# Performance work log

Measured on AMD Instinct MI355X. Metric: run time of the kernel, lower is better.

The kernel has to match this reference:

```python
import jax, jax.numpy as jnp
import numpy as np

GRID = 512
F_FEAT = 32
CORE = 16
N_PTS = 2097152
SCALE = 0.1


def _bilinear_sample(plane, coords):
    """plane: (F, H, W); coords: (N, 2) with (x, y) in [-1, 1], align_corners=True.
    Returns (F, N)."""
    F_, H, W = plane.shape
    x = (coords[:, 0] + 1.0) * 0.5 * (W - 1)
    y = (coords[:, 1] + 1.0) * 0.5 * (H - 1)
    x0f = jnp.floor(x)
    y0f = jnp.floor(y)
    wx = x - x0f  # (N,)
    wy = y - y0f
    x0 = jnp.clip(x0f.astype(jnp.int32), 0, W - 1)
    x1 = jnp.clip(x0 + 1, 0, W - 1)
    y0 = jnp.clip(y0f.astype(jnp.int32), 0, H - 1)
    y1 = jnp.clip(y0 + 1, 0, H - 1)
    v00 = plane[:, y0, x0]  # (F, N)
    v01 = plane[:, y0, x1]
    v10 = plane[:, y1, x0]
    v11 = plane[:, y1, x1]
    return (v00 * (1.0 - wx) * (1.0 - wy)
            + v01 * wx * (1.0 - wy)
            + v10 * (1.0 - wx) * wy
            + v11 * wx * wy)


def setup_inputs() -> dict:
    key = jax.random.key(0)
    k1, k2, k3, k4, k5 = jax.random.split(key, 5)
    coords_plane = jax.random.uniform(
        k1, (3, 1, N_PTS, 1, 2), dtype=jnp.float32, minval=-1.0, maxval=1.0)
    plane_xy = SCALE * jax.random.normal(k2, (1, F_FEAT, GRID, GRID), dtype=jnp.float32)
    plane_yz = SCALE * jax.random.normal(k3, (1, F_FEAT, GRID, GRID), dtype=jnp.float32)
    plane_xz = SCALE * jax.random.normal(k4, (1, F_FEAT, GRID, GRID), dtype=jnp.float32)
    core_tensor = jax.random.normal(k5, (CORE, F_FEAT), dtype=jnp.float32)
    return {"coords_plane": coords_plane, "plane_xy": plane_xy,
            "plane_yz": plane_yz, "plane_xz": plane_xz,
            "core_tensor": core_tensor}


def reference(coords_plane, plane_xy, plane_yz, plane_xz, core_tensor):
    # coords_plane: (3, 1, N, 1, 2) -> (3, N, 2)
    c = coords_plane.reshape(3, -1, 2)
    f_xy = _bilinear_sample(plane_xy[0], c[0])  # (F, N)
    f_yz = _bilinear_sample(plane_yz[0], c[1])
    f_xz = _bilinear_sample(plane_xz[0], c[2])
    prod = f_xy * f_yz * f_xz                   # (F, N)
    # sum over core dim: out[f, n] = (sum_k core[k, f]) * prod[f, n]
    scale = jnp.sum(core_tensor, axis=0)        # (F,)
    out = (scale[:, None] * prod).T             # (N, F)
    return out
```

## Files before the change

kernel.cpp:

```cpp
#include <hip/hip_runtime.h>
#include <hip/hip_fp16.h>

#define N_PTS 2097152
#define GRID_ 512
#define F_FEAT 32
#define HW (GRID_ * GRID_)
#define HWF ((size_t)HW * F_FEAT)

#define NBINS 64
#define BIN_SHIFT 3
#define BIN_CAP 36864
#define CUR_STRIDE 32
#define PTS_PER_BLOCK 1024
#define SEGCAP 64
#define BPB 288

typedef float f32x4 __attribute__((ext_vector_type(4)));
typedef unsigned long long u64;

__global__ void td_scale_kernel(const float* __restrict__ core,
                                float* __restrict__ scale) {
    int f = threadIdx.x;
    float s = 0.0f;
#pragma unroll
    for (int k = 0; k < 16; ++k) s += core[k * F_FEAT + f];
    scale[f] = s;
}

__global__ void td_transpose_kernel(const float* __restrict__ pxy,
                                    const float* __restrict__ pyz,
                                    const float* __restrict__ pxz,
                                    const float* __restrict__ scale,
                                    __half* __restrict__ wsh) {
    __shared__ float tile[32][33];
    const int plane = blockIdx.z;
    const float* src = (plane == 0) ? pxy : ((plane == 1) ? pyz : pxz);
    __half* dst = wsh + (size_t)plane * HWF;
    const int y = blockIdx.y;
    const int x0 = blockIdx.x * 32;

    for (int i = threadIdx.y; i < 32; i += 8) {
        tile[i][threadIdx.x] =
            src[(size_t)i * HW + (size_t)y * GRID_ + x0 + threadIdx.x];
    }
    __syncthreads();
    const float sc = (plane == 0) ? scale[threadIdx.x] : 1.0f;
    for (int i = threadIdx.y; i < 32; i += 8) {
        dst[((size_t)(y * GRID_ + x0 + i)) * F_FEAT + threadIdx.x] =
            __float2half(tile[threadIdx.x][i] * sc);
    }
}

__global__ void td_zero_kernel(int* __restrict__ cursor) {
    for (int i = threadIdx.x; i < 3 * NBINS * CUR_STRIDE; i += 256) cursor[i] = 0;
}

__global__ __launch_bounds__(256) void td_bin_kernel(
    const float2* __restrict__ coords, int* __restrict__ cursor,
    u64* __restrict__ recs) {
    __shared__ int lhist[NBINS];
    __shared__ int lbase[NBINS];
    __shared__ u64 lseg[NBINS][SEGCAP];
    const int pl = blockIdx.y;
    const int tid = threadIdx.x;
    const int base_p = blockIdx.x * PTS_PER_BLOCK;
    if (tid < NBINS) lhist[tid] = 0;
    __syncthreads();

    u64 myrec[4];
    int mybin[4], myslot[4];
#pragma unroll
    for (int k = 0; k < 4; ++k) {
        const int p = base_p + k * 256 + tid;
        const float2 c = coords[(size_t)pl * N_PTS + p];
        const float xf = (c.x + 1.0f) * 0.5f * (float)(GRID_ - 1);
        const float yf = (c.y + 1.0f) * 0.5f * (float)(GRID_ - 1);
        const float x0f = floorf(xf);
        const float y0f = floorf(yf);
        const float wx = xf - x0f;
        const float wy = yf - y0f;
        int x0 = min(max((int)x0f, 0), GRID_ - 1);
        int y0 = min(max((int)y0f, 0), GRID_ - 1);
        const int qwx = min(4095, (int)(wx * 4096.0f + 0.5f));
        const int qwy = min(4095, (int)(wy * 4096.0f + 0.5f));
        const int bin = y0 >> BIN_SHIFT;
        myrec[k] = (u64)p | ((u64)x0 << 21) | ((u64)y0 << 30) |
                   ((u64)qwx << 39) | ((u64)qwy << 51);
        mybin[k] = bin;
        myslot[k] = atomicAdd(&lhist[bin], 1);
    }
    __syncthreads();

    if (tid < NBINS) {
        const int cnt = lhist[tid];
        lbase[tid] =
            (cnt > 0)
                ? atomicAdd(&cursor[(pl * NBINS + tid) * CUR_STRIDE], cnt)
                : 0;
    }
#pragma unroll
    for (int k = 0; k < 4; ++k)
        if (myslot[k] < SEGCAP) lseg[mybin[k]][myslot[k]] = myrec[k];
    __syncthreads();

#pragma unroll
    for (int k = 0; k < 4; ++k) {
        if (myslot[k] >= SEGCAP) {
            const int gslot = lbase[mybin[k]] + myslot[k];
            if (gslot < BIN_CAP)
                recs[((size_t)pl * NBINS + mybin[k]) * BIN_CAP + gslot] =
                    myrec[k];
        }
    }
    for (int b = 0; b < NBINS; ++b) {
        const int cnt = min(lhist[b], SEGCAP);
        const int gb = lbase[b];
        for (int r = tid; r < cnt; r += 256) {
            if (gb + r < BIN_CAP)
                recs[((size_t)pl * NBINS + b) * BIN_CAP + gb + r] = lseg[b][r];
        }
    }
}

__device__ __forceinline__ int td_bin_of_block(int i, int* sub) {
    const int xcd = i & 7;
    const int j = i >> 3;
    const int g = j / BPB;
    *sub = j - g * BPB;
    return g * 8 + xcd;
}

__global__ __launch_bounds__(256) void td_sample_binned_kernel(
    const u64* __restrict__ recs, const int* __restrict__ cursor,
    const f32x4* __restrict__ ws4, f32x4* __restrict__ feat) {
    const int pl = blockIdx.y;
    int sub;
    const int bin = td_bin_of_block(blockIdx.x, &sub);
    const int fq = threadIdx.x & 3;
    const int s0 = sub * 128 + (threadIdx.x >> 2);
    const int cnt = min(cursor[(pl * NBINS + bin) * CUR_STRIDE], BIN_CAP);
    if (s0 >= cnt) return;
    const bool has2 = (s0 + 64) < cnt;

    const size_t rbase = ((size_t)pl * NBINS + bin) * BIN_CAP;
    const f32x4* tp = ws4 + (size_t)pl * (HWF / 8);

    const u64 r0 = __builtin_nontemporal_load(&recs[rbase + s0]);
    const u64 r1 =
        has2 ? __builtin_nontemporal_load(&recs[rbase + s0 + 64]) : r0;

    int pid[2];
    size_t idx[2][4];
    float w[2][4];
    const u64 rr[2] = {r0, r1};
#pragma unroll
    for (int t = 0; t < 2; ++t) {
        const u64 r = rr[t];
        pid[t] = (int)(r & 0x1FFFFF);
        const int x0 = (int)((r >> 21) & 511);
        const int y0 = (int)((r >> 30) & 511);
        const float wx = (float)((int)((r >> 39) & 4095)) * (1.0f / 4096.0f);
        const float wy = (float)((int)((r >> 51) & 4095)) * (1.0f / 4096.0f);
        const int x1 = min(x0 + 1, GRID_ - 1);
        const int y1 = min(y0 + 1, GRID_ - 1);
        idx[t][0] = (size_t)(y0 * GRID_ + x0) * 4 + fq;
        idx[t][1] = (size_t)(y0 * GRID_ + x1) * 4 + fq;
        idx[t][2] = (size_t)(y1 * GRID_ + x0) * 4 + fq;
        idx[t][3] = (size_t)(y1 * GRID_ + x1) * 4 + fq;
        w[t][0] = (1.0f - wx) * (1.0f - wy);
        w[t][1] = wx * (1.0f - wy);
        w[t][2] = (1.0f - wx) * wy;
        w[t][3] = wx * wy;
    }

    f32x4 v[2][4];
#pragma unroll
    for (int t = 0; t < 2; ++t)
#pragma unroll
        for (int c = 0; c < 4; ++c) v[t][c] = tp[idx[t][c]];

#pragma unroll
    for (int t = 0; t < 2; ++t) {
        if (t == 1 && !has2) break;
        const half2* h0 = reinterpret_cast<const half2*>(&v[t][0]);
        const half2* h1 = reinterpret_cast<const half2*>(&v[t][1]);
        const half2* h2 = reinterpret_cast<const half2*>(&v[t][2]);
        const half2* h3 = reinterpret_cast<const half2*>(&v[t][3]);
        union {
            f32x4 vv;
            half2 h[4];
        } u;
#pragma unroll
        for (int j = 0; j < 4; ++j) {
            const float2 f00 = __half22float2(h0[j]);
            const float2 f01 = __half22float2(h1[j]);
            const float2 f10 = __half22float2(h2[j]);
            const float2 f11 = __half22float2(h3[j]);
            const float sa = f00.x * w[t][0] + f01.x * w[t][1] +
                             f10.x * w[t][2] + f11.x * w[t][3];
            const float sb = f00.y * w[t][0] + f01.y * w[t][1] +
                             f10.y * w[t][2] + f11.y * w[t][3];
            u.h[j] = __floats2half2_rn(sa, sb);
        }
        __builtin_nontemporal_store(u.vv,
                                    &feat[(size_t)pid[t] * 12 + pl * 4 + fq]);
    }
}

__global__ __launch_bounds__(256) void td_combine_stream_kernel(
    const f32x4* __restrict__ feat, f32x4* __restrict__ out) {
    const size_t t = (size_t)blockIdx.x * 256 + threadIdx.x;
    const size_t pid = t >> 2;
    const int fq = (int)(t & 3);

    union U {
        f32x4 v;
        half2 h[4];
    };
    U a, b, c;
    a.v = __builtin_nontemporal_load(&feat[pid * 12 + fq]);
    b.v = __builtin_nontemporal_load(&feat[pid * 12 + 4 + fq]);
    c.v = __builtin_nontemporal_load(&feat[pid * 12 + 8 + fq]);

    float rr[8];
#pragma unroll
    for (int j = 0; j < 4; ++j) {
        const float2 fa = __half22float2(a.h[j]);
        const float2 fb = __half22float2(b.h[j]);
        const float2 fc = __half22float2(c.h[j]);
        rr[2 * j] = fa.x * fb.x * fc.x;
        rr[2 * j + 1] = fa.y * fb.y * fc.y;
    }
    f32x4 o0, o1;
    o0.x = rr[0]; o0.y = rr[1]; o0.z = rr[2]; o0.w = rr[3];
    o1.x = rr[4]; o1.y = rr[5]; o1.z = rr[6]; o1.w = rr[7];
    __builtin_nontemporal_store(o0, &out[pid * 8 + fq * 2]);
    __builtin_nontemporal_store(o1, &out[pid * 8 + fq * 2 + 1]);
}

__global__ __launch_bounds__(256) void td_sample_kernel(
    const float2* __restrict__ coords, const f32x4* __restrict__ ws4,
    f32x4* __restrict__ out) {
    const int tid = blockIdx.x * 256 + threadIdx.x;
    const int p = tid >> 2;
    const int fq = tid & 3;

    const float2 c0 = coords[p];
    const float2 c1 = coords[N_PTS + p];
    const float2 c2 = coords[2 * N_PTS + p];

    size_t idx[3][4];
    float w[3][4];
    const float2 cc[3] = {c0, c1, c2};
#pragma unroll
    for (int pl = 0; pl < 3; ++pl) {
        const float xf = (cc[pl].x + 1.0f) * 0.5f * (float)(GRID_ - 1);
        const float yf = (cc[pl].y + 1.0f) * 0.5f * (float)(GRID_ - 1);
        const float x0f = floorf(xf);
        const float y0f = floorf(yf);
        const float wx = xf - x0f;
        const float wy = yf - y0f;
        int x0 = min(max((int)x0f, 0), GRID_ - 1);
        int y0 = min(max((int)y0f, 0), GRID_ - 1);
        const int x1 = min(x0 + 1, GRID_ - 1);
        const int y1 = min(y0 + 1, GRID_ - 1);
        const size_t base = (size_t)pl * (HWF / 8);
        idx[pl][0] = base + (size_t)(y0 * GRID_ + x0) * 4 + fq;
        idx[pl][1] = base + (size_t)(y0 * GRID_ + x1) * 4 + fq;
        idx[pl][2] = base + (size_t)(y1 * GRID_ + x0) * 4 + fq;
        idx[pl][3] = base + (size_t)(y1 * GRID_ + x1) * 4 + fq;
        w[pl][0] = (1.0f - wx) * (1.0f - wy);
        w[pl][1] = wx * (1.0f - wy);
        w[pl][2] = (1.0f - wx) * wy;
        w[pl][3] = wx * wy;
    }

    f32x4 v[3][4];
#pragma unroll
    for (int pl = 0; pl < 3; ++pl)
#pragma unroll
        for (int cnr = 0; cnr < 4; ++cnr) v[pl][cnr] = ws4[idx[pl][cnr]];

    float prod[8];
#pragma unroll
    for (int j = 0; j < 8; ++j) prod[j] = 1.0f;
#pragma unroll
    for (int pl = 0; pl < 3; ++pl) {
        const half2* h0 = reinterpret_cast<const half2*>(&v[pl][0]);
        const half2* h1 = reinterpret_cast<const half2*>(&v[pl][1]);
        const half2* h2 = reinterpret_cast<const half2*>(&v[pl][2]);
        const half2* h3 = reinterpret_cast<const half2*>(&v[pl][3]);
#pragma unroll
        for (int j = 0; j < 4; ++j) {
            const float2 f00 = __half22float2(h0[j]);
            const float2 f01 = __half22float2(h1[j]);
            const float2 f10 = __half22float2(h2[j]);
            const float2 f11 = __half22float2(h3[j]);
            prod[2 * j] *= f00.x * w[pl][0] + f01.x * w[pl][1] +
                           f10.x * w[pl][2] + f11.x * w[pl][3];
            prod[2 * j + 1] *= f00.y * w[pl][0] + f01.y * w[pl][1] +
                               f10.y * w[pl][2] + f11.y * w[pl][3];
        }
    }

    f32x4 o0, o1;
    o0.x = prod[0]; o0.y = prod[1]; o0.z = prod[2]; o0.w = prod[3];
    o1.x = prod[4]; o1.y = prod[5]; o1.z = prod[6]; o1.w = prod[7];
    __builtin_nontemporal_store(o0, &out[(size_t)tid * 2]);
    __builtin_nontemporal_store(o1, &out[(size_t)tid * 2 + 1]);
}

__global__ __launch_bounds__(256) void td_fallback_kernel(
    const float* __restrict__ coords, const float* __restrict__ pxy,
    const float* __restrict__ pyz, const float* __restrict__ pxz,
    const float* __restrict__ core, float* __restrict__ out) {
    const int tid = blockIdx.x * 256 + threadIdx.x;
    const int p = tid >> 5;
    const int f = tid & 31;

    float s = 0.0f;
#pragma unroll
    for (int k = 0; k < 16; ++k) s += core[k * F_FEAT + f];

    float prod = s;
    const float* planes[3] = {pxy, pyz, pxz};
#pragma unroll
    for (int plane = 0; plane < 3; ++plane) {
        const float cx = coords[((size_t)plane * N_PTS + p) * 2 + 0];
        const float cy = coords[((size_t)plane * N_PTS + p) * 2 + 1];
        const float xf = (cx + 1.0f) * 0.5f * (float)(GRID_ - 1);
        const float yf = (cy + 1.0f) * 0.5f * (float)(GRID_ - 1);
        const float x0f = floorf(xf);
        const float y0f = floorf(yf);
        const float wx = xf - x0f;
        const float wy = yf - y0f;
        int x0 = min(max((int)x0f, 0), GRID_ - 1);
        int y0 = min(max((int)y0f, 0), GRID_ - 1);
        const int x1 = min(x0 + 1, GRID_ - 1);
        const int y1 = min(y0 + 1, GRID_ - 1);
        const float* src = planes[plane] + (size_t)f * HW;
        const float v00 = src[y0 * GRID_ + x0];
        const float v01 = src[y0 * GRID_ + x1];
        const float v10 = src[y1 * GRID_ + x0];
        const float v11 = src[y1 * GRID_ + x1];
        prod *= v00 * (1.0f - wx) * (1.0f - wy) + v01 * wx * (1.0f - wy) +
                v10 * (1.0f - wx) * wy + v11 * wx * wy;
    }
    out[(size_t)p * F_FEAT + f] = prod;
}

extern "C" void kernel_launch(void* const* d_in, const int* in_sizes, int n_in,
                              void* d_out, int out_size, void* d_ws,
                              size_t ws_size, hipStream_t stream) {
    const float* coords = (const float*)d_in[0];
    const float* pxy = (const float*)d_in[1];
    const float* pyz = (const float*)d_in[2];
    const float* pxz = (const float*)d_in[3];
    const float* core = (const float*)d_in[4];
    float* out = (float*)d_out;

    size_t off = 0;
    auto alloc = [&off](size_t bytes) {
        size_t o = off;
        off = (off + bytes + 255) & ~(size_t)255;
        return o;
    };
    const size_t off_wsh = alloc(3 * HWF * sizeof(__half));
    const size_t off_scale = alloc(32 * sizeof(float));
    const size_t need_r4 = off;
    const size_t off_cur = alloc((size_t)3 * NBINS * CUR_STRIDE * sizeof(int));
    const size_t off_recs = alloc((size_t)3 * NBINS * BIN_CAP * sizeof(u64));
    const size_t off_feat = alloc((size_t)N_PTS * 192);
    const size_t need_full = off;

    char* ws = (char*)d_ws;

    if (ws_size >= need_r4) {
        __half* wsh = (__half*)(ws + off_wsh);
        float* scale = (float*)(ws + off_scale);
        td_scale_kernel<<<1, 32, 0, stream>>>(core, scale);
        td_transpose_kernel<<<dim3(GRID_ / 32, GRID_, 3), dim3(32, 8), 0,
                              stream>>>(pxy, pyz, pxz, scale, wsh);
        if (ws_size >= need_full) {
            int* cursor = (int*)(ws + off_cur);
            u64* recs = (u64*)(ws + off_recs);
            f32x4* feat = (f32x4*)(ws + off_feat);
            td_zero_kernel<<<1, 256, 0, stream>>>(cursor);
            td_bin_kernel<<<dim3(N_PTS / PTS_PER_BLOCK, 3), 256, 0, stream>>>(
                (const float2*)coords, cursor, recs);
            td_sample_binned_kernel<<<dim3(NBINS * BPB, 3), 256, 0, stream>>>(
                recs, cursor, (const f32x4*)wsh, feat);
            td_combine_stream_kernel<<<N_PTS * 4 / 256, 256, 0, stream>>>(
                (const f32x4*)feat, (f32x4*)out);
        } else {
            td_sample_kernel<<<N_PTS * 4 / 256, 256, 0, stream>>>(
                (const float2*)coords, (const f32x4*)wsh, (f32x4*)out);
        }
    } else {
        td_fallback_kernel<<<N_PTS * 32 / 256, 256, 0, stream>>>(
            coords, pxy, pyz, pxz, core, out);
    }
}
```

Before: 375.2 us.

## Stage bin records in shared memory and sample four points per thread

The bin kernel drops its shared-memory segment staging and writes every record straight to its global slot. The sampling kernel now loads 256 records per block into shared memory with one coalesced load, then each quad of threads processes four points instead of two, with the blocks-per-bin count halved to match. This aims to raise memory-level parallelism per thread (16 gathers in flight) and cut block count, at the cost of more registers and possibly lower occupancy. It also makes the bin kernel's global writes scattered rather than grouped per bin.

Result: faster. 365.8 us (-2.5%).

```diff
diff --git a/kernel.cpp b/kernel.cpp
--- a/kernel.cpp
+++ b/kernel.cpp
@@ -12,8 +12,8 @@
 #define BIN_CAP 36864
 #define CUR_STRIDE 32
 #define PTS_PER_BLOCK 1024
-#define SEGCAP 64
-#define BPB 288
+#define SLOTS_PER_BLOCK 256
+#define BPB 144
 
 typedef float f32x4 __attribute__((ext_vector_type(4)));
 typedef unsigned long long u64;
@@ -60,7 +60,6 @@
     u64* __restrict__ recs) {
     __shared__ int lhist[NBINS];
     __shared__ int lbase[NBINS];
-    __shared__ u64 lseg[NBINS][SEGCAP];
     const int pl = blockIdx.y;
     const int tid = threadIdx.x;
     const int base_p = blockIdx.x * PTS_PER_BLOCK;
@@ -98,27 +97,13 @@
                 ? atomicAdd(&cursor[(pl * NBINS + tid) * CUR_STRIDE], cnt)
                 : 0;
     }
-#pragma unroll
-    for (int k = 0; k < 4; ++k)
-        if (myslot[k] < SEGCAP) lseg[mybin[k]][myslot[k]] = myrec[k];
     __syncthreads();
 
 #pragma unroll
     for (int k = 0; k < 4; ++k) {
-        if (myslot[k] >= SEGCAP) {
-            const int gslot = lbase[mybin[k]] + myslot[k];
-            if (gslot < BIN_CAP)
-                recs[((size_t)pl * NBINS + mybin[k]) * BIN_CAP + gslot] =
-                    myrec[k];
-        }
-    }
-    for (int b = 0; b < NBINS; ++b) {
-        const int cnt = min(lhist[b], SEGCAP);
-        const int gb = lbase[b];
-        for (int r = tid; r < cnt; r += 256) {
-            if (gb + r < BIN_CAP)
-                recs[((size_t)pl * NBINS + b) * BIN_CAP + gb + r] = lseg[b][r];
-        }
+        const int gslot = lbase[mybin[k]] + myslot[k];
+        if (gslot < BIN_CAP)
+            recs[((size_t)pl * NBINS + mybin[k]) * BIN_CAP + gslot] = myrec[k];
     }
 }
 
@@ -133,34 +118,45 @@
 __global__ __launch_bounds__(256) void td_sample_binned_kernel(
     const u64* __restrict__ recs, const int* __restrict__ cursor,
     const f32x4* __restrict__ ws4, f32x4* __restrict__ feat) {
+    __shared__ u64 srecs[SLOTS_PER_BLOCK];
     const int pl = blockIdx.y;
     int sub;
     const int bin = td_bin_of_block(blockIdx.x, &sub);
-    const int fq = threadIdx.x & 3;
-    const int s0 = sub * 128 + (threadIdx.x >> 2);
+    const int tid = threadIdx.x;
+    const int fq = tid & 3;
+    const int q = tid >> 2;
     const int cnt = min(cursor[(pl * NBINS + bin) * CUR_STRIDE], BIN_CAP);
-    if (s0 >= cnt) return;
-    const bool has2 = (s0 + 64) < cnt;
+    const int sbase = sub * SLOTS_PER_BLOCK;
+    if (sbase >= cnt) return;
 
     const size_t rbase = ((size_t)pl * NBINS + bin) * BIN_CAP;
+    {
+        const int s = sbase + tid;
+        srecs[tid] = recs[rbase + min(s, cnt - 1)];
+    }
+    __syncthreads();
+
     const f32x4* tp = ws4 + (size_t)pl * (HWF / 8);
 
-    const u64 r0 = __builtin_nontemporal_load(&recs[rbase + s0]);
-    const u64 r1 =
-        has2 ? __builtin_nontemporal_load(&recs[rbase + s0 + 64]) : r0;
-
-    int pid[2];
-    size_t idx[2][4];
-    float w[2][4];
-    const u64 rr[2] = {r0, r1};
-#pragma unroll
-    for (int t = 0; t < 2; ++t) {
-        const u64 r = rr[t];
-        pid[t] = (int)(r & 0x1FFFFF);
-        const int x0 = (int)((r >> 21) & 511);
-        const int y0 = (int)((r >> 30) & 511);
-        const float wx = (float)((int)((r >> 39) & 4095)) * (1.0f / 4096.0f);
-        const float wy = (float)((int)((r >> 51) & 4095)) * (1.0f / 4096.0f);
+    u64 r[4];
+    bool act[4];
+#pragma unroll
+    for (int t = 0; t < 4; ++t) {
+        const int ls = q + t * 64;
+        act[t] = (sbase + ls) < cnt;
+        r[t] = srecs[act[t] ? ls : 0];
+    }
+
+    int pid[4];
+    size_t idx[4][4];
+    float w[4][4];
+#pragma unroll
+    for (int t = 0; t < 4; ++t) {
+        pid[t] = (int)(r[t] & 0x1FFFFF);
+        const int x0 = (int)((r[t] >> 21) & 511);
+        const int y0 = (int)((r[t] >> 30) & 511);
+        const float wx = (float)((int)((r[t] >> 39) & 4095)) * (1.0f / 4096.0f);
+        const float wy = (float)((int)((r[t] >> 51) & 4095)) * (1.0f / 4096.0f);
         const int x1 = min(x0 + 1, GRID_ - 1);
         const int y1 = min(y0 + 1, GRID_ - 1);
         idx[t][0] = (size_t)(y0 * GRID_ + x0) * 4 + fq;
@@ -173,15 +169,15 @@
         w[t][3] = wx * wy;
     }
 
-    f32x4 v[2][4];
-#pragma unroll
-    for (int t = 0; t < 2; ++t)
+    f32x4 v[4][4];
+#pragma unroll
+    for (int t = 0; t < 4; ++t)
 #pragma unroll
         for (int c = 0; c < 4; ++c) v[t][c] = tp[idx[t][c]];
 
 #pragma unroll
-    for (int t = 0; t < 2; ++t) {
-        if (t == 1 && !has2) break;
+    for (int t = 0; t < 4; ++t) {
+        if (!act[t]) continue;
         const half2* h0 = reinterpret_cast<const half2*>(&v[t][0]);
         const half2* h1 = reinterpret_cast<const half2*>(&v[t][1]);
         const half2* h2 = reinterpret_cast<const half2*>(&v[t][2]);
```
